# Optimization experiments

Hardware: AMD Instinct MI355X
Metric: run time of the kernel (lower is better)

Reference implementation:

```python
import jax, jax.numpy as jnp
import numpy as np

GN_EPS = 1e-5
NUM_GROUPS = 32


def setup_inputs() -> dict:
    key = jax.random.key(0)
    ks = jax.random.split(key, 4)
    B, K, N = 8192, 2048, 4096
    bound = 1.0 / np.sqrt(K)
    return {
        "x": jax.random.normal(ks[0], (B, K), dtype=jnp.float32),
        "weight": jax.random.normal(ks[1], (N, K), dtype=jnp.float32) * bound,
        "bias_lin": jax.random.uniform(ks[2], (N,), dtype=jnp.float32, minval=-bound, maxval=bound),
        "bias_extra": jax.random.normal(ks[3], (N,), dtype=jnp.float32),
        "gn_weight": jnp.ones((N,), dtype=jnp.float32),
        "gn_bias": jnp.zeros((N,), dtype=jnp.float32),
    }


def reference(x, weight, bias_lin, bias_extra, gn_weight, gn_bias):
    # Fused GEMM + bias + Swish + extra bias:  y = swish(x @ W.T + b_lin) + b_ex
    z = jnp.einsum("bk,nk->bn", x, weight) + bias_lin          # [B, N]
    y = z * jax.nn.sigmoid(z) + bias_extra                      # Swish + extra bias
    # GroupNorm over channel groups
    B, N = y.shape
    G = NUM_GROUPS
    yg = y.reshape(B, G, N // G)
    mean = jnp.mean(yg, axis=2, keepdims=True)
    var = jnp.mean(jnp.square(yg - mean), axis=2, keepdims=True)  # biased variance
    y_norm = ((yg - mean) * jax.lax.rsqrt(var + GN_EPS)).reshape(B, N)
    return y_norm * gn_weight + gn_bias
```

## Files before the change

kernel.cpp:

```cpp
#include <hip/hip_runtime.h>


typedef __attribute__((ext_vector_type(8))) short short8;
typedef __attribute__((ext_vector_type(4))) float f32x4;

#define M_DIM 8192
#define N_DIM 4096
#define K_DIM 2048
#define BM 256
#define BN 256
#define BK 64
#define NT (K_DIM / BK)

__global__ void f32_to_bf16_k(const float* __restrict__ in, ushort* __restrict__ out, int n8) {
    int i = blockIdx.x * blockDim.x + threadIdx.x;
    if (i >= n8) return;
    const float4* p = (const float4*)in + 2 * (size_t)i;
    float4 a = p[0], b = p[1];
    float v[8] = {a.x, a.y, a.z, a.w, b.x, b.y, b.z, b.w};
    ushort rr[8];
#pragma unroll
    for (int j = 0; j < 8; ++j) {
        unsigned u = __float_as_uint(v[j]);
        rr[j] = (ushort)((u + 0x7fffu + ((u >> 16) & 1u)) >> 16);
    }
    uint4 o;
    o.x = (unsigned)rr[0] | ((unsigned)rr[1] << 16);
    o.y = (unsigned)rr[2] | ((unsigned)rr[3] << 16);
    o.z = (unsigned)rr[4] | ((unsigned)rr[5] << 16);
    o.w = (unsigned)rr[6] | ((unsigned)rr[7] << 16);
    ((uint4*)out)[i] = o;
}


#define BAR() __builtin_amdgcn_s_barrier()
#define LGKM0() do { asm volatile("s_waitcnt lgkmcnt(0)" ::: "memory"); __builtin_amdgcn_sched_barrier(0); } while (0)
#define VMC(n_) do { asm volatile("s_waitcnt vmcnt(" #n_ ")" ::: "memory"); __builtin_amdgcn_sched_barrier(0); } while (0)

__global__ __launch_bounds__(512, 2) void gemm_swish_gn(
    const ushort* __restrict__ xb, const ushort* __restrict__ wb,
    const float* __restrict__ bias_lin, const float* __restrict__ bias_extra,
    const float* __restrict__ gn_w, const float* __restrict__ gn_b,
    float* __restrict__ out)
{
    extern __shared__ __align__(16) ushort lds[];

    const int t = threadIdx.x;
    const int w = t >> 6;
    const int l = t & 63;
    const int wm = w >> 2;
    const int wn = w & 3;
    const int h = l >> 4;
    const int r = l & 15;

    const int bid = blockIdx.x;
    const int id = (bid & 7) * 64 + (bid >> 3);
    const int brow = id & 31;
    const int bcol = id >> 5;

    const ushort* pA0 = xb + (size_t)(brow * BM + (t >> 2)) * K_DIM + (t & 3) * 8;
    const ushort* pA1 = pA0 + (size_t)128 * K_DIM;
    const ushort* pB0 = wb + (size_t)(bcol * BN + (t >> 2)) * K_DIM + (t & 3) * 8;
    const ushort* pB1 = pB0 + (size_t)128 * K_DIM;
    const int dst0 = t * 8;

#define STAGE_A(slotU) do {                                                   \
    __builtin_amdgcn_global_load_lds(                                         \
        (const __attribute__((address_space(1))) void*)pA0,                   \
        (__attribute__((address_space(3))) void*)&lds[(slotU) + dst0], 16, 0, 0); \
    __builtin_amdgcn_global_load_lds(                                         \
        (const __attribute__((address_space(1))) void*)pA1,                   \
        (__attribute__((address_space(3))) void*)&lds[(slotU) + 4096 + dst0], 16, 0, 0); \
    pA0 += 32; pA1 += 32; } while (0)

#define STAGE_B(slotU) do {                                                   \
    __builtin_amdgcn_global_load_lds(                                         \
        (const __attribute__((address_space(1))) void*)pB0,                   \
        (__attribute__((address_space(3))) void*)&lds[(slotU) + dst0], 16, 0, 0); \
    __builtin_amdgcn_global_load_lds(                                         \
        (const __attribute__((address_space(1))) void*)pB1,                   \
        (__attribute__((address_space(3))) void*)&lds[(slotU) + 4096 + dst0], 16, 0, 0); \
    pB0 += 32; pB1 += 32; } while (0)

    const int aIdx = (wm * 128 + r) * 32 + h * 8;
    const int bIdx = (wn * 64 + r) * 32 + h * 8;

    f32x4 acc[8][4];
#pragma unroll
    for (int m = 0; m < 8; ++m)
#pragma unroll
        for (int n = 0; n < 4; ++n)
            acc[m][n] = f32x4{0.f, 0.f, 0.f, 0.f};

    STAGE_A(0);
    STAGE_B(16384);
    STAGE_A(8192);
    STAGE_B(24576);
    STAGE_A(32768 + 0);
    STAGE_B(32768 + 16384);
    VMC(8);
    BAR();

    short8 aF[8], bF[4];

#define DO_TILE(P, tt)                                                              \
  {                                                                                 \
                                                    \
    _Pragma("unroll") for (int m = 0; m < 8; ++m)                                   \
        aF[m] = *(const short8*)&lds[(P) * 32768 + aIdx + m * 512];                 \
    bF[0] = *(const short8*)&lds[(P) * 32768 + 16384 + bIdx];                       \
    bF[1] = *(const short8*)&lds[(P) * 32768 + 16384 + bIdx + 512];                 \
    if ((tt) != NT - 1) STAGE_A(((P) ^ 1) * 32768 + 8192);                          \
    BAR(); LGKM0();                                                                 \
    __builtin_amdgcn_s_setprio(1);                                                  \
    _Pragma("unroll") for (int m = 0; m < 8; ++m) {                                 \
        acc[m][0] = __builtin_amdgcn_mfma_f32_16x16x32_bf16(aF[m], bF[0], acc[m][0], 0, 0, 0); \
        acc[m][1] = __builtin_amdgcn_mfma_f32_16x16x32_bf16(aF[m], bF[1], acc[m][1], 0, 0, 0); \
    }                                                                               \
    __builtin_amdgcn_s_setprio(0);                                                  \
    BAR();                                                                          \
                                                    \
    bF[2] = *(const short8*)&lds[(P) * 32768 + 16384 + bIdx + 1024];                \
    bF[3] = *(const short8*)&lds[(P) * 32768 + 16384 + bIdx + 1536];                \
    if ((tt) != NT - 1) STAGE_B(((P) ^ 1) * 32768 + 24576);                         \
    BAR(); LGKM0();                                                                 \
    __builtin_amdgcn_s_setprio(1);                                                  \
    _Pragma("unroll") for (int m = 0; m < 8; ++m) {                                 \
        acc[m][2] = __builtin_amdgcn_mfma_f32_16x16x32_bf16(aF[m], bF[2], acc[m][2], 0, 0, 0); \
        acc[m][3] = __builtin_amdgcn_mfma_f32_16x16x32_bf16(aF[m], bF[3], acc[m][3], 0, 0, 0); \
    }                                                                               \
    __builtin_amdgcn_s_setprio(0);                                                  \
    if ((tt) == NT - 1) { VMC(0); } else { VMC(8); }                                \
    BAR();                                                                          \
                                                    \
    _Pragma("unroll") for (int m = 0; m < 8; ++m)                                   \
        aF[m] = *(const short8*)&lds[(P) * 32768 + 8192 + aIdx + m * 512];          \
    bF[0] = *(const short8*)&lds[(P) * 32768 + 24576 + bIdx];                       \
    bF[1] = *(const short8*)&lds[(P) * 32768 + 24576 + bIdx + 512];                 \
    if ((tt) < NT - 2) STAGE_A((P) * 32768 + 0);                                    \
    BAR(); LGKM0();                                                                 \
    __builtin_amdgcn_s_setprio(1);                                                  \
    _Pragma("unroll") for (int m = 0; m < 8; ++m) {                                 \
        acc[m][0] = __builtin_amdgcn_mfma_f32_16x16x32_bf16(aF[m], bF[0], acc[m][0], 0, 0, 0); \
        acc[m][1] = __builtin_amdgcn_mfma_f32_16x16x32_bf16(aF[m], bF[1], acc[m][1], 0, 0, 0); \
    }                                                                               \
    __builtin_amdgcn_s_setprio(0);                                                  \
    BAR();                                                                          \
                                                    \
    bF[2] = *(const short8*)&lds[(P) * 32768 + 24576 + bIdx + 1024];                \
    bF[3] = *(const short8*)&lds[(P) * 32768 + 24576 + bIdx + 1536];                \
    if ((tt) < NT - 2) STAGE_B((P) * 32768 + 16384);                                \
    BAR(); LGKM0();                                                                 \
    __builtin_amdgcn_s_setprio(1);                                                  \
    _Pragma("unroll") for (int m = 0; m < 8; ++m) {                                 \
        acc[m][2] = __builtin_amdgcn_mfma_f32_16x16x32_bf16(aF[m], bF[2], acc[m][2], 0, 0, 0); \
        acc[m][3] = __builtin_amdgcn_mfma_f32_16x16x32_bf16(aF[m], bF[3], acc[m][3], 0, 0, 0); \
    }                                                                               \
    __builtin_amdgcn_s_setprio(0);                                                  \
    if ((tt) == NT - 2) { VMC(4); } else if ((tt) < NT - 2) { VMC(8); }             \
    BAR();                                                                          \
  }

#pragma unroll 1
    for (int tp = 0; tp < NT; tp += 2) {
        DO_TILE(0, tp);
        DO_TILE(1, tp + 1);
    }

    const int colbase = bcol * BN + wn * 64;
    float bl[4], be[4], gwv[4], gbv[4];
#pragma unroll
    for (int n = 0; n < 4; ++n) {
        int col = colbase + n * 16 + r;
        bl[n] = bias_lin[col];
        be[n] = bias_extra[col];
        gwv[n] = gn_w[col];
        gbv[n] = gn_b[col];
    }

    float s1[8][4], s2[8][4];
#pragma unroll
    for (int m = 0; m < 8; ++m)
#pragma unroll
        for (int j = 0; j < 4; ++j) { s1[m][j] = 0.f; s2[m][j] = 0.f; }

#pragma unroll
    for (int m = 0; m < 8; ++m)
#pragma unroll
        for (int n = 0; n < 4; ++n)
#pragma unroll
            for (int j = 0; j < 4; ++j) {
                float z = acc[m][n][j] + bl[n];
                float sw = z / (1.f + __expf(-z)) + be[n];
                acc[m][n][j] = sw;
                s1[m][j] += sw;
                s2[m][j] += sw * sw;
            }

#pragma unroll
    for (int mask = 1; mask < 16; mask <<= 1) {
#pragma unroll
        for (int m = 0; m < 8; ++m)
#pragma unroll
            for (int j = 0; j < 4; ++j) {
                s1[m][j] += __shfl_xor(s1[m][j], mask, 16);
                s2[m][j] += __shfl_xor(s2[m][j], mask, 16);
            }
    }

    float* sred = (float*)lds;
    const int gh = wn >> 1;
    const int p = wn & 1;
    if (r == 0) {
#pragma unroll
        for (int m = 0; m < 8; ++m)
#pragma unroll
            for (int j = 0; j < 4; ++j) {
                int row = wm * 128 + m * 16 + h * 4 + j;
                sred[((0 * 2 + gh) * 2 + p) * 256 + row] = s1[m][j];
                sred[((1 * 2 + gh) * 2 + p) * 256 + row] = s2[m][j];
            }
    }
    __syncthreads();

    const size_t orow0 = (size_t)brow * BM;
#pragma unroll
    for (int m = 0; m < 8; ++m)
#pragma unroll
        for (int j = 0; j < 4; ++j) {
            int row = wm * 128 + m * 16 + h * 4 + j;
            float mu = (sred[((0 * 2 + gh) * 2 + 0) * 256 + row] +
                        sred[((0 * 2 + gh) * 2 + 1) * 256 + row]) * (1.f / 128.f);
            float ex2 = (sred[((1 * 2 + gh) * 2 + 0) * 256 + row] +
                         sred[((1 * 2 + gh) * 2 + 1) * 256 + row]) * (1.f / 128.f);
            float var = ex2 - mu * mu;
            float rs = rsqrtf(var + 1e-5f);
            float* orow = out + (orow0 + row) * N_DIM;
#pragma unroll
            for (int n = 0; n < 4; ++n) {
                int col = colbase + n * 16 + r;
                orow[col] = (acc[m][n][j] - mu) * rs * gwv[n] + gbv[n];
            }
        }
}

extern "C" void kernel_launch(void* const* d_in, const int* in_sizes, int n_in,
                              void* d_out, int out_size, void* d_ws, size_t ws_size,
                              hipStream_t stream) {
    const float* x        = (const float*)d_in[0];
    const float* weight   = (const float*)d_in[1];
    const float* bias_lin = (const float*)d_in[2];
    const float* bias_ex  = (const float*)d_in[3];
    const float* gn_w     = (const float*)d_in[4];
    const float* gn_b     = (const float*)d_in[5];
    float* out = (float*)d_out;

    ushort* xb = (ushort*)d_ws;
    ushort* wb = xb + (size_t)M_DIM * K_DIM;

    {
        int n8 = (M_DIM * K_DIM) / 8;
        f32_to_bf16_k<<<n8 / 256, 256, 0, stream>>>(x, xb, n8);
    }
    {
        int n8 = (N_DIM * K_DIM) / 8;
        f32_to_bf16_k<<<n8 / 256, 256, 0, stream>>>(weight, wb, n8);
    }

    (void)hipFuncSetAttribute((const void*)gemm_swish_gn,
                              hipFuncAttributeMaxDynamicSharedMemorySize, 131072);

    dim3 grid((M_DIM / BM) * (N_DIM / BN));
    gemm_swish_gn<<<grid, 512, 131072, stream>>>(xb, wb, bias_lin, bias_ex, gn_w, gn_b, out);
}
```

Measured before the change: 206.5 us.

## Use XOR-swizzled full-BK LDS layout and reorder quadrant MFMA schedule

Replaces the two half-K (32-wide) sub-tiles per stage with a single 64-wide K row layout in LDS, using an XOR swizzle on 16-byte chunks to avoid bank conflicts on ds_read. The main loop now processes a full BK tile per DO_TILE in four quadrants (m 0-3/4-7 × n 0-1/2-3), loading both K halves per fragment and interleaving the prefetch of the next stage into the other buffer. It aims to cut LDS bank conflicts and halve register fragment pressure for A, at the cost of a more intricate wait-count and barrier schedule.

```diff
diff --git a/kernel.cpp b/kernel.cpp
--- a/kernel.cpp
+++ b/kernel.cpp
@@ -12,6 +12,9 @@
 #define BK 64
 #define NT (K_DIM / BK)
 
+#define AS1 __attribute__((address_space(1)))
+#define AS3 __attribute__((address_space(3)))
+
 __global__ void f32_to_bf16_k(const float* __restrict__ in, ushort* __restrict__ out, int n8) {
     int i = blockIdx.x * blockDim.x + threadIdx.x;
     if (i >= n8) return;
@@ -58,32 +61,26 @@
     const int brow = id & 31;
     const int bcol = id >> 5;
 
-    const ushort* pA0 = xb + (size_t)(brow * BM + (t >> 2)) * K_DIM + (t & 3) * 8;
-    const ushort* pA1 = pA0 + (size_t)128 * K_DIM;
-    const ushort* pB0 = wb + (size_t)(bcol * BN + (t >> 2)) * K_DIM + (t & 3) * 8;
-    const ushort* pB1 = pB0 + (size_t)128 * K_DIM;
-    const int dst0 = t * 8;
-
-#define STAGE_A(slotU) do {                                                   \
-    __builtin_amdgcn_global_load_lds(                                         \
-        (const __attribute__((address_space(1))) void*)pA0,                   \
-        (__attribute__((address_space(3))) void*)&lds[(slotU) + dst0], 16, 0, 0); \
-    __builtin_amdgcn_global_load_lds(                                         \
-        (const __attribute__((address_space(1))) void*)pA1,                   \
-        (__attribute__((address_space(3))) void*)&lds[(slotU) + 4096 + dst0], 16, 0, 0); \
-    pA0 += 32; pA1 += 32; } while (0)
-
-#define STAGE_B(slotU) do {                                                   \
-    __builtin_amdgcn_global_load_lds(                                         \
-        (const __attribute__((address_space(1))) void*)pB0,                   \
-        (__attribute__((address_space(3))) void*)&lds[(slotU) + dst0], 16, 0, 0); \
-    __builtin_amdgcn_global_load_lds(                                         \
-        (const __attribute__((address_space(1))) void*)pB1,                   \
-        (__attribute__((address_space(3))) void*)&lds[(slotU) + 4096 + dst0], 16, 0, 0); \
-    pB0 += 32; pB1 += 32; } while (0)
-
-    const int aIdx = (wm * 128 + r) * 32 + h * 8;
-    const int bIdx = (wn * 64 + r) * 32 + h * 8;
+    const int s = t >> 3;
+    const int scol = (((t & 7) ^ (s & 7)) << 3);
+    const ushort* pA = xb + (size_t)(brow * BM + s) * K_DIM + scol;
+    const int rB = (s & 31) + ((s >> 5) << 6);
+    const ushort* pB = wb + (size_t)(bcol * BN + rB) * K_DIM + scol;
+    const int dstA = t * 8;
+    const int dstB = rB * 64 + ((t & 7) << 3);
+
+#define STG_A(P, ROFF) __builtin_amdgcn_global_load_lds(                         \
+        (const AS1 void*)(pA + (size_t)(ROFF) * K_DIM),                          \
+        (AS3 void*)&lds[(P) * 32768 + (ROFF) * 64 + dstA], 16, 0, 0)
+#define STG_B(P, ROFF) __builtin_amdgcn_global_load_lds(                         \
+        (const AS1 void*)(pB + (size_t)(ROFF) * K_DIM),                          \
+        (AS3 void*)&lds[(P) * 32768 + 16384 + (ROFF) * 64 + dstB], 16, 0, 0)
+
+    const int xr8 = (r & 7) << 3;
+    const int aOff0 = (wm * 128 + r) * 64 + ((h << 3) ^ xr8);
+    const int aOff1 = aOff0 ^ 32;
+    const int bOff0 = 16384 + (wn * 64 + r) * 64 + ((h << 3) ^ xr8);
+    const int bOff1 = bOff0 ^ 32;
 
     f32x4 acc[8][4];
 #pragma unroll
@@ -92,72 +89,78 @@
         for (int n = 0; n < 4; ++n)
             acc[m][n] = f32x4{0.f, 0.f, 0.f, 0.f};
 
-    STAGE_A(0);
-    STAGE_B(16384);
-    STAGE_A(8192);
-    STAGE_B(24576);
-    STAGE_A(32768 + 0);
-    STAGE_B(32768 + 16384);
-    VMC(8);
+    STG_A(0, 0); STG_A(0, 128);
+    STG_A(0, 64); STG_A(0, 192);
+    STG_B(0, 0); STG_B(0, 128);
+    STG_B(0, 32); STG_B(0, 160);
+    pA += BK; pB += BK;
+    VMC(2);
     BAR();
 
-    short8 aF[8], bF[4];
+    short8 aF[4][2], bF[4][2];
+
+#define MFMA(mm, nn, kk, ai) \
+    acc[mm][nn] = __builtin_amdgcn_mfma_f32_16x16x32_bf16(aF[ai][kk], bF[nn][kk], acc[mm][nn], 0, 0, 0)
 
 #define DO_TILE(P, tt)                                                              \
   {                                                                                 \
                                                     \
-    _Pragma("unroll") for (int m = 0; m < 8; ++m)                                   \
-        aF[m] = *(const short8*)&lds[(P) * 32768 + aIdx + m * 512];                 \
-    bF[0] = *(const short8*)&lds[(P) * 32768 + 16384 + bIdx];                       \
-    bF[1] = *(const short8*)&lds[(P) * 32768 + 16384 + bIdx + 512];                 \
-    if ((tt) != NT - 1) STAGE_A(((P) ^ 1) * 32768 + 8192);                          \
-    BAR(); LGKM0();                                                                 \
-    __builtin_amdgcn_s_setprio(1);                                                  \
-    _Pragma("unroll") for (int m = 0; m < 8; ++m) {                                 \
-        acc[m][0] = __builtin_amdgcn_mfma_f32_16x16x32_bf16(aF[m], bF[0], acc[m][0], 0, 0, 0); \
-        acc[m][1] = __builtin_amdgcn_mfma_f32_16x16x32_bf16(aF[m], bF[1], acc[m][1], 0, 0, 0); \
-    }                                                                               \
-    __builtin_amdgcn_s_setprio(0);                                                  \
+    _Pragma("unroll") for (int m = 0; m < 4; ++m) {                                 \
+        aF[m][0] = *(const short8*)&lds[(P) * 32768 + aOff0 + m * 1024];            \
+        aF[m][1] = *(const short8*)&lds[(P) * 32768 + aOff1 + m * 1024];            \
+    }                                                                               \
+    _Pragma("unroll") for (int n = 0; n < 2; ++n) {                                 \
+        bF[n][0] = *(const short8*)&lds[(P) * 32768 + bOff0 + n * 1024];            \
+        bF[n][1] = *(const short8*)&lds[(P) * 32768 + bOff1 + n * 1024];            \
+    }                                                                               \
+    if ((tt) != NT - 1) { STG_A(P ^ 1, 0); STG_A(P ^ 1, 128); }                     \
+    BAR(); LGKM0();                                                                 \
+    __builtin_amdgcn_s_setprio(1);                                                  \
+    _Pragma("unroll") for (int m = 0; m < 4; ++m)                                   \
+        _Pragma("unroll") for (int n = 0; n < 2; ++n) {                             \
+            MFMA(m, n, 0, m); MFMA(m, n, 1, m);                                     \
+        }                                                                           \
+    __builtin_amdgcn_s_setprio(0);                                                  \
+    if ((tt) == NT - 1) { VMC(0); } else { VMC(2); }                                \
     BAR();                                                                          \
                                                     \
-    bF[2] = *(const short8*)&lds[(P) * 32768 + 16384 + bIdx + 1024];                \
-    bF[3] = *(const short8*)&lds[(P) * 32768 + 16384 + bIdx + 1536];                \
-    if ((tt) != NT - 1) STAGE_B(((P) ^ 1) * 32768 + 24576);                         \
-    BAR(); LGKM0();                                                                 \
-    __builtin_amdgcn_s_setprio(1);                                                  \
-    _Pragma("unroll") for (int m = 0; m < 8; ++m) {                                 \
-        acc[m][2] = __builtin_amdgcn_mfma_f32_16x16x32_bf16(aF[m], bF[2], acc[m][2], 0, 0, 0); \
-        acc[m][3] = __builtin_amdgcn_mfma_f32_16x16x32_bf16(aF[m], bF[3], acc[m][3], 0, 0, 0); \
-    }                                                                               \
-    __builtin_amdgcn_s_setprio(0);                                                  \
-    if ((tt) == NT - 1) { VMC(0); } else { VMC(8); }                                \
-    BAR();                                                                          \
-                                                    \
-    _Pragma("unroll") for (int m = 0; m < 8; ++m)                                   \
-        aF[m] = *(const short8*)&lds[(P) * 32768 + 8192 + aIdx + m * 512];          \
-    bF[0] = *(const short8*)&lds[(P) * 32768 + 24576 + bIdx];                       \
-    bF[1] = *(const short8*)&lds[(P) * 32768 + 24576 + bIdx + 512];                 \
-    if ((tt) < NT - 2) STAGE_A((P) * 32768 + 0);                                    \
-    BAR(); LGKM0();                                                                 \
-    __builtin_amdgcn_s_setprio(1);                                                  \
-    _Pragma("unroll") for (int m = 0; m < 8; ++m) {                                 \
-        acc[m][0] = __builtin_amdgcn_mfma_f32_16x16x32_bf16(aF[m], bF[0], acc[m][0], 0, 0, 0); \
-        acc[m][1] = __builtin_amdgcn_mfma_f32_16x16x32_bf16(aF[m], bF[1], acc[m][1], 0, 0, 0); \
-    }                                                                               \
-    __builtin_amdgcn_s_setprio(0);                                                  \
-    BAR();                                                                          \
-                                                    \
-    bF[2] = *(const short8*)&lds[(P) * 32768 + 24576 + bIdx + 1024];                \
-    bF[3] = *(const short8*)&lds[(P) * 32768 + 24576 + bIdx + 1536];                \
-    if ((tt) < NT - 2) STAGE_B((P) * 32768 + 16384);                                \
-    BAR(); LGKM0();                                                                 \
-    __builtin_amdgcn_s_setprio(1);                                                  \
-    _Pragma("unroll") for (int m = 0; m < 8; ++m) {                                 \
-        acc[m][2] = __builtin_amdgcn_mfma_f32_16x16x32_bf16(aF[m], bF[2], acc[m][2], 0, 0, 0); \
-        acc[m][3] = __builtin_amdgcn_mfma_f32_16x16x32_bf16(aF[m], bF[3], acc[m][3], 0, 0, 0); \
-    }                                                                               \
-    __builtin_amdgcn_s_setprio(0);                                                  \
-    if ((tt) == NT - 2) { VMC(4); } else if ((tt) < NT - 2) { VMC(8); }             \
+    _Pragma("unroll") for (int n = 2; n < 4; ++n) {                                 \
+        bF[n][0] = *(const short8*)&lds[(P) * 32768 + bOff0 + n * 1024];            \
+        bF[n][1] = *(const short8*)&lds[(P) * 32768 + bOff1 + n * 1024];            \
+    }                                                                               \
+    if ((tt) != NT - 1) { STG_A(P ^ 1, 64); STG_A(P ^ 1, 192); }                    \
+    BAR(); LGKM0();                                                                 \
+    __builtin_amdgcn_s_setprio(1);                                                  \
+    _Pragma("unroll") for (int m = 0; m < 4; ++m)                                   \
+        _Pragma("unroll") for (int n = 2; n < 4; ++n) {                             \
+            MFMA(m, n, 0, m); MFMA(m, n, 1, m);                                     \
+        }                                                                           \
+    __builtin_amdgcn_s_setprio(0);                                                  \
+    BAR();                                                                          \
+                                   \
+    _Pragma("unroll") for (int m = 4; m < 8; ++m) {                                 \
+        aF[m - 4][0] = *(const short8*)&lds[(P) * 32768 + aOff0 + m * 1024];        \
+        aF[m - 4][1] = *(const short8*)&lds[(P) * 32768 + aOff1 + m * 1024];        \
+    }                                                                               \
+    if ((tt) != NT - 1) { STG_B(P ^ 1, 0); STG_B(P ^ 1, 128); }                     \
+    BAR(); LGKM0();                                                                 \
+    __builtin_amdgcn_s_setprio(1);                                                  \
+    _Pragma("unroll") for (int m = 4; m < 8; ++m)                                   \
+        _Pragma("unroll") for (int n = 0; n < 2; ++n) {                             \
+            MFMA(m, n, 0, m - 4); MFMA(m, n, 1, m - 4);                             \
+        }                                                                           \
+    __builtin_amdgcn_s_setprio(0);                                                  \
+    BAR();                                                                          \
+                                    \
+    if ((tt) != NT - 1) { STG_B(P ^ 1, 32); STG_B(P ^ 1, 160); pA += BK; pB += BK; } \
+    BAR(); LGKM0();                                                                 \
+    __builtin_amdgcn_s_setprio(1);                                                  \
+    _Pragma("unroll") for (int m = 4; m < 8; ++m)                                   \
+        _Pragma("unroll") for (int n = 2; n < 4; ++n) {                             \
+            MFMA(m, n, 0, m - 4); MFMA(m, n, 1, m - 4);                             \
+        }                                                                           \
+    __builtin_amdgcn_s_setprio(0);                                                  \
+    if ((tt) < NT - 1) { VMC(2); }                                                  \
     BAR();                                                                          \
   }
 
```

Measured after the change: 191.1 us. 1.08x faster.
